# Optimization experiments

Hardware: AMD Instinct MI355X
Metric: run time of the kernel (lower is better)

Reference implementation:

```python
import jax, jax.numpy as jnp
import numpy as np

B, T, V, E, H, K, PAD = 32, 512, 50000, 256, 512, 17, 0


def setup_inputs() -> dict:
    key = jax.random.key(0)
    ks = jax.random.split(key, 16)
    s = 0.05
    input_ids = jax.random.randint(ks[0], (B, T), 1, V)
    lengths = jax.random.randint(ks[1], (B,), T // 2, T + 1)  # >=1 token, mask[:,0] all True
    tags = jax.random.randint(ks[2], (B, T), 0, K)
    mask = jnp.arange(T)[None, :] < lengths[:, None]
    emb = (jax.random.normal(ks[3], (V, E)) * s).at[PAD].set(0.0)  # padding_idx row zeroed
    w_ih_f = jax.random.normal(ks[4], (4 * H, E)) * s
    w_hh_f = jax.random.normal(ks[5], (4 * H, H)) * s
    b_f = jax.random.normal(ks[6], (4 * H,)) * s
    w_ih_b = jax.random.normal(ks[7], (4 * H, E)) * s
    w_hh_b = jax.random.normal(ks[8], (4 * H, H)) * s
    b_b = jax.random.normal(ks[9], (4 * H,)) * s
    w_cls = jax.random.normal(ks[10], (K, 2 * H)) * s
    b_cls = jax.random.normal(ks[11], (K,)) * s
    start_trans = jax.random.normal(ks[12], (K,)) * s
    trans = jax.random.normal(ks[13], (K, K)) * s
    end_trans = jax.random.normal(ks[14], (K,)) * s
    return dict(input_ids=input_ids, lengths=lengths, tags=tags, mask=mask,
                emb=emb, w_ih_f=w_ih_f, w_hh_f=w_hh_f, b_f=b_f,
                w_ih_b=w_ih_b, w_hh_b=w_hh_b, b_b=b_b,
                w_cls=w_cls, b_cls=b_cls,
                start_trans=start_trans, trans=trans, end_trans=end_trans)


def _lstm(xg, w_hh):
    # xg: [B,T,4H] = x @ W_ih^T + b (precomputed); scan adds recurrent term.
    Bq, Hq = xg.shape[0], w_hh.shape[1]

    def step(carry, g_in):
        h, c = carry
        g = g_in + h @ w_hh.T
        i, f, gg, o = jnp.split(g, 4, axis=-1)  # torch gate order i,f,g,o
        c = jax.nn.sigmoid(f) * c + jax.nn.sigmoid(i) * jnp.tanh(gg)
        h = jax.nn.sigmoid(o) * jnp.tanh(c)
        return (h, c), h

    init = (jnp.zeros((Bq, Hq), xg.dtype), jnp.zeros((Bq, Hq), xg.dtype))
    _, hs = jax.lax.scan(step, init, jnp.swapaxes(xg, 0, 1))
    return jnp.swapaxes(hs, 0, 1)  # [B,T,H]


def _forward_math(input_ids, lengths, tags, mask, emb,
                  w_ih_f, w_hh_f, b_f, w_ih_b, w_hh_b, b_b,
                  w_cls, b_cls, start_trans, trans, end_trans):
    x = emb[input_ids]  # [B,T,E]
    # forward direction over padded seq (valid prefix is causally correct)
    hf = _lstm(x @ w_ih_f.T + b_f, w_hh_f)
    # backward direction: reverse each sequence within its own length (packed semantics)
    t = jnp.arange(input_ids.shape[1])[None, :]
    rev = jnp.where(t < lengths[:, None], lengths[:, None] - 1 - t, t)  # involution on valid region
    xr = jnp.take_along_axis(x, rev[:, :, None], axis=1)
    hb = _lstm(xr @ w_ih_b.T + b_b, w_hh_b)
    hb = jnp.take_along_axis(hb, rev[:, :, None], axis=1)
    enc = jnp.concatenate([hf, hb], axis=-1)  # dropout = identity (eval / p=0)
    emissions = enc @ w_cls.T + b_cls  # [B,T,K]
    m = mask.astype(emissions.dtype)
    # ---- CRF numerator (gold path score) ----
    emis_sc = jnp.sum(jnp.take_along_axis(emissions, tags[:, :, None], axis=2)[..., 0] * m, axis=1)
    tr_sc = jnp.sum(trans[tags[:, :-1], tags[:, 1:]] * m[:, 1:], axis=1)
    last_tag = jnp.take_along_axis(tags, (lengths - 1)[:, None], axis=1)[:, 0]
    numer = start_trans[tags[:, 0]] + emis_sc + tr_sc + end_trans[last_tag]
    # ---- CRF partition (forward algorithm) ----
    def fstep(alpha, inp):
        e_t, m_t = inp
        nxt = jax.nn.logsumexp(alpha[:, :, None] + trans[None, :, :] + e_t[:, None, :], axis=1)
        return jnp.where(m_t[:, None], nxt, alpha), None

    alpha0 = start_trans[None, :] + emissions[:, 0]
    alphaT, _ = jax.lax.scan(
        fstep, alpha0,
        (jnp.swapaxes(emissions[:, 1:], 0, 1), jnp.swapaxes(mask[:, 1:], 0, 1)))
    logZ = jax.nn.logsumexp(alphaT + end_trans[None, :], axis=1)
    return -jnp.mean(numer - logZ)  # reduction='mean', negated


def reference(input_ids, lengths, tags, mask, emb, w_ih_f, w_hh_f, b_f,
              w_ih_b, w_hh_b, b_b, w_cls, b_cls, start_trans, trans, end_trans):
    return _forward_math(input_ids, lengths, tags, mask, emb, w_ih_f, w_hh_f, b_f,
                         w_ih_b, w_hh_b, b_b, w_cls, b_cls, start_trans, trans, end_trans)
```

## Files before the change

### kernel.cpp

```cpp
#include <hip/hip_runtime.h>
#include <hip/hip_bf16.h>
#include <stdint.h>

#define B_  32
#define T_  512
#define E_  256
#define H_  512
#define K_  17

typedef unsigned short us;
typedef __attribute__((ext_vector_type(8))) short short8;
typedef __attribute__((ext_vector_type(4))) float f32x4;

__device__ __forceinline__ float bf2f(unsigned int u16) {
    union { unsigned int i; float f; } v; v.i = u16 << 16; return v.f;
}
__device__ __forceinline__ us f2bf(float f) {
    union { float f; unsigned int i; } v; v.f = f;
    unsigned int b = v.i;
    return (us)((b + 0x7FFFu + ((b >> 16) & 1u)) >> 16);
}
__device__ __forceinline__ float sigf(float x) { return 1.0f / (1.0f + __expf(-x)); }
__device__ __forceinline__ float tanhf_(float x) { return 1.0f - 2.0f / (__expf(2.0f * x) + 1.0f); }

__global__ void k_cvt(const float* __restrict__ src, us* __restrict__ dst, int n4) {
    int i = blockIdx.x * 256 + threadIdx.x;
    if (i < n4) {
        float4 v = ((const float4*)src)[i];
        uint2 p;
        p.x = (uint32_t)f2bf(v.x) | ((uint32_t)f2bf(v.y) << 16);
        p.y = (uint32_t)f2bf(v.z) | ((uint32_t)f2bf(v.w) << 16);
        ((uint2*)dst)[i] = p;
    }
}

__global__ void k_init(const int* __restrict__ ids, const int* __restrict__ lengths,
                       int* __restrict__ ids2, int* __restrict__ marker,
                       int* __restrict__ flags, float* __restrict__ out) {
    int idx = blockIdx.x * 256 + threadIdx.x;
    if (idx == 0) { *marker = 1; out[0] = -3328.0f; }
    if (idx < 1024) flags[idx] = 0;
    if (idx < 2 * B_ * T_) {
        int dir = idx >> 14;
        int r   = idx & 16383;
        int t   = r >> 5;
        int b   = r & 31;
        int l   = lengths[b];
        int tt  = (dir == 0) ? t : ((t < l) ? (l - 1 - t) : t);
        ids2[idx] = ids[b * T_ + tt];
    }
}

__launch_bounds__(256)
__global__ void k_xg(const us* __restrict__ emb,
                     const us* __restrict__ wf, const float* __restrict__ bfv,
                     const us* __restrict__ wb, const float* __restrict__ bbv,
                     const int* __restrict__ ids2, us* __restrict__ xg,
                     int* __restrict__ marker) {
    if (blockIdx.x == 0 && blockIdx.y == 0 && blockIdx.z == 0 && threadIdx.x == 0)
        atomicOr(marker, 2);
    int mt = blockIdx.x, nt = blockIdx.y, dir = blockIdx.z;
    const us* W      = dir ? wb  : wf;
    const float* bias = dir ? bbv : bfv;
    const int* id2 = ids2 + dir * (B_ * T_);
    us* xgd = xg + (size_t)dir * B_ * T_ * 2048;
    int m0 = mt * 64, n0 = nt * 64;
    __shared__ __align__(16) us As[64][136];
    __shared__ __align__(16) us Bs[64][136];
    int tid = threadIdx.x;
    int wv = tid >> 6, lane = tid & 63;
    int lm = lane & 15, lg = lane >> 4;
    f32x4 z = {0.f, 0.f, 0.f, 0.f};
    f32x4 acc[4] = {z, z, z, z};
    for (int half = 0; half < 2; ++half) {
        for (int c = tid; c < 1024; c += 256) {
            int row = c >> 4, cb = c & 15;
            int mg = m0 + row;
            int j = mg >> 2, g = mg & 3;
            *(uint4*)&As[row][cb * 8] =
                *(const uint4*)(W + ((size_t)(g * H_ + j)) * E_ + half * 128 + cb * 8);
            int gi = id2[n0 + row];
            *(uint4*)&Bs[row][cb * 8] =
                *(const uint4*)(emb + (size_t)gi * E_ + half * 128 + cb * 8);
        }
        __syncthreads();
#pragma unroll
        for (int kt = 0; kt < 4; ++kt) {
            short8 a = *(const short8*)&As[wv * 16 + lm][kt * 32 + lg * 8];
#pragma unroll
            for (int n2 = 0; n2 < 4; ++n2) {
                short8 b = *(const short8*)&Bs[n2 * 16 + lm][kt * 32 + lg * 8];
                acc[n2] = __builtin_amdgcn_mfma_f32_16x16x32_bf16(a, b, acc[n2], 0, 0, 0);
            }
        }
        __syncthreads();
    }
    int jgb = m0 + wv * 16 + lg * 4;
    int j = jgb >> 2;
#pragma unroll
    for (int n2 = 0; n2 < 4; ++n2) {
        int token = n0 + n2 * 16 + lm;
        us p[4];
#pragma unroll
        for (int q = 0; q < 4; ++q)
            p[q] = f2bf(acc[n2][q] + bias[q * H_ + j]);
        uint2 pv;
        pv.x = (uint32_t)p[0] | ((uint32_t)p[1] << 16);
        pv.y = (uint32_t)p[2] | ((uint32_t)p[3] << 16);
        *(uint2*)(xgd + (size_t)token * 2048 + jgb) = pv;
    }
}

__launch_bounds__(256)
__global__ void k_lstm(const us* __restrict__ whf, const us* __restrict__ whb,
                       const us* __restrict__ xg,
                       us* __restrict__ h_state, us* __restrict__ h_out,
                       int* __restrict__ flags, int* __restrict__ marker) {
    int bid = blockIdx.x;
    int dir = bid >> 5, w = bid & 31;
    int tid = threadIdx.x;
    if (bid == 0 && tid == 0) atomicOr(marker, 4);
    const us* Wg = dir ? whb : whf;
    __shared__ __align__(16) us Ws[64 * 512];
    __shared__ __align__(4)  us Hx[32 * 16];
    for (int c = tid; c < 4096; c += 256) {
        int row = c >> 6, cb = c & 63;
        int rt = row >> 4, rl = row & 15;
        int jj = rl >> 2, g = rl & 3;
        int srcRow = g * H_ + w * 16 + rt * 4 + jj;
        uint4 v = *(const uint4*)(Wg + (size_t)srcRow * H_ + cb * 8);
        int lb = row * 1024 + ((cb * 16) ^ ((row & 7) << 4));
        *(uint4*)((char*)Ws + lb) = v;
    }
    __syncthreads();
    int wv = tid >> 6, lane = tid & 63;
    int nb = wv & 1, rh = wv >> 1;
    int lm = lane & 15, lg = lane >> 4;
    int b = nb * 16 + lm;
    const us* xgd = xg + (size_t)dir * B_ * T_ * 2048;
    us* hod = h_out + (size_t)dir * B_ * T_ * H_;
    int* slots = flags + dir * 512;
    const uint64_t* hbase = (const uint64_t*)h_state + (size_t)dir * 8192;
    uint32_t* hw32 = (uint32_t*)h_state + (size_t)dir * 16384;
    float cc0 = 0.f, cc1 = 0.f;
    bool alive = true;
#pragma unroll 1
    for (int t = 0; t < T_; ++t) {
        f32x4 acc[2];
#pragma unroll
        for (int ti = 0; ti < 2; ++ti) {
            int jl = rh * 8 + ti * 4 + lg;
            uint2 v = *(const uint2*)(xgd + ((size_t)(t * 32 + b)) * 2048 + (w * 16 + jl) * 4);
            acc[ti][0] = bf2f(v.x & 0xffff); acc[ti][1] = bf2f(v.x >> 16);
            acc[ti][2] = bf2f(v.y & 0xffff); acc[ti][3] = bf2f(v.y >> 16);
        }
        if (t > 0) {
            if (wv == 0) {
                int polls = 0;
                for (;;) {
                    int v = (lane < 32)
                        ? __hip_atomic_load(&slots[lane * 16], __ATOMIC_RELAXED, __HIP_MEMORY_SCOPE_AGENT)
                        : 0x7fffffff;
                    if (__all(v >= t) || !alive) break;
                    __builtin_amdgcn_s_sleep(1);
                    if (++polls > 300000) {
                        if (lane == 0) atomicOr(marker, 32);
                        alive = false;
                    }
                }
            }
            __syncthreads();
            const uint64_t* hp = hbase + ((t - 1) & 1) * 4096 + (size_t)b * 128 + lg * 2;
            uint64_t hv[32];
#pragma unroll
            for (int kt = 0; kt < 16; ++kt) {
                hv[2 * kt]     = __hip_atomic_load(hp + kt * 8,     __ATOMIC_RELAXED, __HIP_MEMORY_SCOPE_AGENT);
                hv[2 * kt + 1] = __hip_atomic_load(hp + kt * 8 + 1, __ATOMIC_RELAXED, __HIP_MEMORY_SCOPE_AGENT);
            }
#pragma unroll
            for (int ti = 0; ti < 2; ++ti) {
                int r0 = (rh * 2 + ti) * 16 + lm;
                const char* abase = (const char*)Ws + r0 * 1024;
                int sw = (r0 & 7) << 4;
#pragma unroll
                for (int kt = 0; kt < 16; ++kt) {
                    union { uint64_t u[2]; short8 s; } bu;
                    bu.u[0] = hv[2 * kt]; bu.u[1] = hv[2 * kt + 1];
                    short8 a = *(const short8*)(abase + ((kt * 64 + lg * 16) ^ sw));
                    acc[ti] = __builtin_amdgcn_mfma_f32_16x16x32_bf16(a, bu.s, acc[ti], 0, 0, 0);
                }
            }
        }
        {
            float ci = cc0;
            ci = sigf(acc[0][1]) * ci + sigf(acc[0][0]) * tanhf_(acc[0][2]);
            float h = sigf(acc[0][3]) * tanhf_(ci);
            cc0 = ci;
            us hv = f2bf(h);
            int jl = rh * 8 + lg;
            Hx[b * 16 + jl] = hv;
            hod[((size_t)b * T_ + t) * H_ + w * 16 + jl] = hv;
        }
        {
            float ci = cc1;
            ci = sigf(acc[1][1]) * ci + sigf(acc[1][0]) * tanhf_(acc[1][2]);
            float h = sigf(acc[1][3]) * tanhf_(ci);
            cc1 = ci;
            us hv = f2bf(h);
            int jl = rh * 8 + 4 + lg;
            Hx[b * 16 + jl] = hv;
            hod[((size_t)b * T_ + t) * H_ + w * 16 + jl] = hv;
        }
        __syncthreads();
        {
            uint32_t v = ((const uint32_t*)Hx)[tid];
            int bb = tid >> 3, jp = tid & 7;
            atomicExch(&hw32[(size_t)(t & 1) * 8192 + (size_t)bb * 256 + w * 8 + jp], v);
        }
        __syncthreads();
        if (tid == 0) atomicExch(&slots[w * 16], t + 1);
    }
}

__launch_bounds__(256)
__global__ void k_emis(const us* __restrict__ h_out,
                       const us* __restrict__ wcls, const float* __restrict__ bcls,
                       const int* __restrict__ lengths, float* __restrict__ emis,
                       int* __restrict__ marker) {
    if (blockIdx.x == 0 && threadIdx.x == 0) atomicOr(marker, 8);
    __shared__ __align__(8) us Wc[17][1032];
    int tid = threadIdx.x;
    for (int c = tid; c < 17 * 256; c += 256) {
        int row = c >> 8; int c4 = (c & 255) * 4;
        *(uint2*)&Wc[row][c4] = *(const uint2*)(wcls + (size_t)row * 1024 + c4);
    }
    __syncthreads();
    int i = blockIdx.x * 8 + (tid >> 5);
    int k = tid & 31;
    int b = i >> 9, t = i & 511;
    int l = lengths[b];
    int trv = (t < l) ? (l - 1 - t) : t;
    const us* hf = h_out + ((size_t)(0 * B_ + b) * T_ + t) * H_;
    const us* hb = h_out + ((size_t)(1 * B_ + b) * T_ + trv) * H_;
    if (k < K_) {
        float acc = bcls[k];
        for (int e = 0; e < H_; e += 4) {
            uint2 hv = *(const uint2*)(hf + e);
            uint2 wv = *(const uint2*)&Wc[k][e];
            acc = fmaf(bf2f(hv.x & 0xffff), bf2f(wv.x & 0xffff), acc);
            acc = fmaf(bf2f(hv.x >> 16),    bf2f(wv.x >> 16),    acc);
            acc = fmaf(bf2f(hv.y & 0xffff), bf2f(wv.y & 0xffff), acc);
            acc = fmaf(bf2f(hv.y >> 16),    bf2f(wv.y >> 16),    acc);
        }
        for (int e = 0; e < H_; e += 4) {
            uint2 hv = *(const uint2*)(hb + e);
            uint2 wv = *(const uint2*)&Wc[k][512 + e];
            acc = fmaf(bf2f(hv.x & 0xffff), bf2f(wv.x & 0xffff), acc);
            acc = fmaf(bf2f(hv.x >> 16),    bf2f(wv.x >> 16),    acc);
            acc = fmaf(bf2f(hv.y & 0xffff), bf2f(wv.y & 0xffff), acc);
            acc = fmaf(bf2f(hv.y >> 16),    bf2f(wv.y >> 16),    acc);
        }
        emis[(size_t)i * 20 + k] = acc;
    }
}

__global__ void k_crf(const float* __restrict__ emis, const int* __restrict__ tags,
                      const int* __restrict__ lengths,
                      const float* __restrict__ start_t, const float* __restrict__ trans_t,
                      const float* __restrict__ end_t, float* __restrict__ res,
                      int* __restrict__ marker) {
    if (blockIdx.x == 0 && threadIdx.x == 0) atomicOr(marker, 16);
    __shared__ float tr[17][18];
    __shared__ float alpha[17];
    int b = blockIdx.x, tid = threadIdx.x;
    for (int i = tid; i < 289; i += 64) tr[i / 17][i % 17] = trans_t[i];
    __syncthreads();
    int l = lengths[b];
    const int* tg = tags + b * T_;
    const float* eb = emis + (size_t)b * T_ * 20;
    float sn = 0.f;
    for (int t = tid; t < T_; t += 64) {
        if (t < l) {
            sn += eb[t * 20 + tg[t]];
            if (t >= 1) sn += tr[tg[t - 1]][tg[t]];
        }
    }
#pragma unroll
    for (int off = 32; off; off >>= 1) sn += __shfl_xor(sn, off, 64);
    float numer = sn + start_t[tg[0]] + end_t[tg[l - 1]];
    int k = (tid < K_) ? tid : 0;
    if (tid < K_) alpha[tid] = start_t[tid] + eb[tid];
    __syncthreads();
    for (int t = 1; t < l; ++t) {
        float av[17];
        float m = -1e30f;
#pragma unroll
        for (int j = 0; j < 17; ++j) { av[j] = alpha[j] + tr[j][k]; m = fmaxf(m, av[j]); }
        float s = 0.f;
#pragma unroll
        for (int j = 0; j < 17; ++j) s += __expf(av[j] - m);
        float nxt = m + __logf(s) + eb[t * 20 + k];
        __syncthreads();
        if (tid < K_) alpha[tid] = nxt;
        __syncthreads();
    }
    float v = (tid < K_) ? (alpha[tid] + end_t[tid]) : -1e30f;
    float m2 = v;
#pragma unroll
    for (int off = 32; off; off >>= 1) m2 = fmaxf(m2, __shfl_xor(m2, off, 64));
    float s2 = __expf(v - m2);
#pragma unroll
    for (int off = 32; off; off >>= 1) s2 += __shfl_xor(s2, off, 64);
    if (tid == 0) res[b] = numer - (m2 + __logf(s2));
}

__global__ void k_fin(const float* __restrict__ res, int* __restrict__ marker,
                      int hostmask, float* __restrict__ out) {
    int tid = threadIdx.x;
    if (hostmask != 0) {
        if (tid == 0) out[0] = -(16384.0f + 512.0f * (float)hostmask);
        return;
    }
    int dm = atomicOr(marker, 0);
    if (dm != 31) {
        if (tid == 0) out[0] = -(8192.0f + 128.0f * (float)(dm & 63));
        return;
    }
    float v = (tid < B_) ? res[tid] : 0.f;
    unsigned long long nb = __ballot(v != v);
    if (nb != 0ULL) {
        if (tid == 0) out[0] = -(4096.0f + (float)(__ffsll((long long)nb) - 1));
        return;
    }
#pragma unroll
    for (int off = 32; off; off >>= 1) v += __shfl_xor(v, off, 64);
    if (tid == 0) out[0] = -(v / (float)B_);
}

extern "C" void kernel_launch(void* const* d_in, const int* in_sizes, int n_in,
                              void* d_out, int out_size, void* d_ws, size_t ws_size,
                              hipStream_t stream) {
    const int* ids      = (const int*)d_in[0];
    const int* lengths  = (const int*)d_in[1];
    const int* tags     = (const int*)d_in[2];
    const float* emb_f  = (const float*)d_in[4];
    const float* wihf_f = (const float*)d_in[5];
    const float* whhf_f = (const float*)d_in[6];
    const float* bfv    = (const float*)d_in[7];
    const float* wihb_f = (const float*)d_in[8];
    const float* whhb_f = (const float*)d_in[9];
    const float* bbv    = (const float*)d_in[10];
    const float* wcls_f = (const float*)d_in[11];
    const float* bcls   = (const float*)d_in[12];
    const float* start  = (const float*)d_in[13];
    const float* trans  = (const float*)d_in[14];
    const float* endt   = (const float*)d_in[15];
    float* out = (float*)d_out;

    int hm = 0;
    if (n_in != 16 || out_size != 1) hm |= 8;
    const int exp_sz[16] = {
        16384, 32, 16384, 16384,
        12800000,
        524288, 1048576, 2048,
        524288, 1048576, 2048,
        17408, 17,
        17, 289, 17
    };
    if (!(hm & 8))
        for (int i = 0; i < 16; ++i)
            if (in_sizes[i] != exp_sz[i]) hm |= 2;

    char* w = (char*)d_ws;
    size_t off = 0;
    auto carve = [&](size_t bytes) { void* p = w + off; off += (bytes + 255) & ~(size_t)255; return p; };
    int* ids2    = (int*)carve((size_t)2 * B_ * T_ * 4);
    int* marker  = (int*)carve(256);
    int* flags   = (int*)carve(4096);
    float* res   = (float*)carve(256);
    float* emis  = (float*)carve((size_t)B_ * T_ * 20 * 4);
    us* xg       = (us*)carve((size_t)2 * B_ * T_ * 2048 * 2);
    us* h_st     = (us*)carve((size_t)2 * 2 * B_ * H_ * 2);
    us* h_out    = (us*)carve((size_t)2 * B_ * T_ * H_ * 2);
    us* emb_b    = (us*)carve((size_t)12800000 * 2);
    us* wihf_b   = (us*)carve((size_t)524288 * 2);
    us* wihb_b   = (us*)carve((size_t)524288 * 2);
    us* whhf_b   = (us*)carve((size_t)1048576 * 2);
    us* whhb_b   = (us*)carve((size_t)1048576 * 2);
    us* wcls_b   = (us*)carve((size_t)17408 * 2);
    if (off > ws_size) hm |= 4;

    (void)hipGetLastError();
    if ((hm & (2 | 4 | 8)) == 0) {
        k_init<<<(2 * B_ * T_ + 255) / 256, 256, 0, stream>>>(ids, lengths, ids2, marker, flags, out);
        k_cvt<<<(12800000 / 4 + 255) / 256, 256, 0, stream>>>(emb_f,  emb_b,  12800000 / 4);
        k_cvt<<<(524288   / 4 + 255) / 256, 256, 0, stream>>>(wihf_f, wihf_b, 524288 / 4);
        k_cvt<<<(524288   / 4 + 255) / 256, 256, 0, stream>>>(wihb_f, wihb_b, 524288 / 4);
        k_cvt<<<(1048576  / 4 + 255) / 256, 256, 0, stream>>>(whhf_f, whhf_b, 1048576 / 4);
        k_cvt<<<(1048576  / 4 + 255) / 256, 256, 0, stream>>>(whhb_f, whhb_b, 1048576 / 4);
        k_cvt<<<(17408    / 4 + 255) / 256, 256, 0, stream>>>(wcls_f, wcls_b, 17408 / 4);
        k_xg<<<dim3(2048 / 64, B_ * T_ / 64, 2), 256, 0, stream>>>(emb_b, wihf_b, bfv, wihb_b, bbv, ids2, xg, marker);
        k_lstm<<<64, 256, 0, stream>>>(whhf_b, whhb_b, xg, h_st, h_out, flags, marker);
        k_emis<<<B_ * T_ / 8, 256, 0, stream>>>(h_out, wcls_b, bcls, lengths, emis, marker);
        k_crf<<<B_, 64, 0, stream>>>(emis, tags, lengths, start, trans, endt, res, marker);
        if (hipGetLastError() != hipSuccess) hm |= 1;
    }
    k_fin<<<1, 64, 0, stream>>>(res, marker, hm, out);
}
```

Measured before the change: 3.066 ms.

## Cut per-step barriers in LSTM handoff and CRF recurrence using shuffles

In the persistent LSTM kernel, the shared-memory staging buffer and one of the two block barriers per timestep are removed. Lanes pair adjacent bf16 outputs through a wave shuffle and publish them straight to the global h exchange buffer with relaxed atomic stores. The flag update becomes a release store, and the xg gate-input loads are issued before the poll/wait so their latency overlaps it. The CRF forward recurrence keeps alpha in registers, broadcast by shuffle, with transition columns in registers, which removes two barriers per step. The risk is that memory ordering now rests on the release store after a single barrier.

After: 3.896 ms. +27.1%, slower.

```diff
diff --git a/kernel.cpp b/kernel.cpp
--- a/kernel.cpp
+++ b/kernel.cpp
@@ -122,7 +122,6 @@
     if (bid == 0 && tid == 0) atomicOr(marker, 4);
     const us* Wg = dir ? whb : whf;
     __shared__ __align__(16) us Ws[64 * 512];
-    __shared__ __align__(4)  us Hx[32 * 16];
     for (int c = tid; c < 4096; c += 256) {
         int row = c >> 6, cb = c & 63;
         int rt = row >> 4, rl = row & 15;
@@ -137,6 +136,8 @@
     int nb = wv & 1, rh = wv >> 1;
     int lm = lane & 15, lg = lane >> 4;
     int b = nb * 16 + lm;
+    int jl0 = rh * 8 + lg;
+    int jl1 = rh * 8 + 4 + lg;
     const us* xgd = xg + (size_t)dir * B_ * T_ * 2048;
     us* hod = h_out + (size_t)dir * B_ * T_ * H_;
     int* slots = flags + dir * 512;
@@ -146,14 +147,9 @@
     bool alive = true;
 #pragma unroll 1
     for (int t = 0; t < T_; ++t) {
+        uint2 vr0 = *(const uint2*)(xgd + ((size_t)(t * 32 + b)) * 2048 + (w * 16 + jl0) * 4);
+        uint2 vr1 = *(const uint2*)(xgd + ((size_t)(t * 32 + b)) * 2048 + (w * 16 + jl1) * 4);
         f32x4 acc[2];
-#pragma unroll
-        for (int ti = 0; ti < 2; ++ti) {
-            int jl = rh * 8 + ti * 4 + lg;
-            uint2 v = *(const uint2*)(xgd + ((size_t)(t * 32 + b)) * 2048 + (w * 16 + jl) * 4);
-            acc[ti][0] = bf2f(v.x & 0xffff); acc[ti][1] = bf2f(v.x >> 16);
-            acc[ti][2] = bf2f(v.y & 0xffff); acc[ti][3] = bf2f(v.y >> 16);
-        }
         if (t > 0) {
             if (wv == 0) {
                 int polls = 0;
@@ -177,6 +173,10 @@
                 hv[2 * kt]     = __hip_atomic_load(hp + kt * 8,     __ATOMIC_RELAXED, __HIP_MEMORY_SCOPE_AGENT);
                 hv[2 * kt + 1] = __hip_atomic_load(hp + kt * 8 + 1, __ATOMIC_RELAXED, __HIP_MEMORY_SCOPE_AGENT);
             }
+            acc[0][0] = bf2f(vr0.x & 0xffff); acc[0][1] = bf2f(vr0.x >> 16);
+            acc[0][2] = bf2f(vr0.y & 0xffff); acc[0][3] = bf2f(vr0.y >> 16);
+            acc[1][0] = bf2f(vr1.x & 0xffff); acc[1][1] = bf2f(vr1.x >> 16);
+            acc[1][2] = bf2f(vr1.y & 0xffff); acc[1][3] = bf2f(vr1.y >> 16);
 #pragma unroll
             for (int ti = 0; ti < 2; ++ti) {
                 int r0 = (rh * 2 + ti) * 16 + lm;
@@ -190,35 +190,31 @@
                     acc[ti] = __builtin_amdgcn_mfma_f32_16x16x32_bf16(a, bu.s, acc[ti], 0, 0, 0);
                 }
             }
-        }
-        {
-            float ci = cc0;
-            ci = sigf(acc[0][1]) * ci + sigf(acc[0][0]) * tanhf_(acc[0][2]);
-            float h = sigf(acc[0][3]) * tanhf_(ci);
-            cc0 = ci;
-            us hv = f2bf(h);
-            int jl = rh * 8 + lg;
-            Hx[b * 16 + jl] = hv;
-            hod[((size_t)b * T_ + t) * H_ + w * 16 + jl] = hv;
-        }
-        {
-            float ci = cc1;
-            ci = sigf(acc[1][1]) * ci + sigf(acc[1][0]) * tanhf_(acc[1][2]);
-            float h = sigf(acc[1][3]) * tanhf_(ci);
-            cc1 = ci;
-            us hv = f2bf(h);
-            int jl = rh * 8 + 4 + lg;
-            Hx[b * 16 + jl] = hv;
-            hod[((size_t)b * T_ + t) * H_ + w * 16 + jl] = hv;
+        } else {
+            acc[0][0] = bf2f(vr0.x & 0xffff); acc[0][1] = bf2f(vr0.x >> 16);
+            acc[0][2] = bf2f(vr0.y & 0xffff); acc[0][3] = bf2f(vr0.y >> 16);
+            acc[1][0] = bf2f(vr1.x & 0xffff); acc[1][1] = bf2f(vr1.x >> 16);
+            acc[1][2] = bf2f(vr1.y & 0xffff); acc[1][3] = bf2f(vr1.y >> 16);
+        }
+        cc0 = sigf(acc[0][1]) * cc0 + sigf(acc[0][0]) * tanhf_(acc[0][2]);
+        float h0 = sigf(acc[0][3]) * tanhf_(cc0);
+        cc1 = sigf(acc[1][1]) * cc1 + sigf(acc[1][0]) * tanhf_(acc[1][2]);
+        float h1 = sigf(acc[1][3]) * tanhf_(cc1);
+        us p0 = f2bf(h0), p1 = f2bf(h1);
+        hod[((size_t)b * T_ + t) * H_ + w * 16 + jl0] = p0;
+        hod[((size_t)b * T_ + t) * H_ + w * 16 + jl1] = p1;
+        int y0 = __shfl((int)p0, lane + 16);
+        int y1 = __shfl((int)p1, lane + 16);
+        if ((lg & 1) == 0) {
+            uint32_t u0 = (uint32_t)p0 | ((uint32_t)(us)y0 << 16);
+            uint32_t u1 = (uint32_t)p1 | ((uint32_t)(us)y1 << 16);
+            uint32_t* hwp = hw32 + (size_t)(t & 1) * 8192 + (size_t)b * 256 + w * 8 + rh * 4 + (lg >> 1);
+            __hip_atomic_store(hwp,     u0, __ATOMIC_RELAXED, __HIP_MEMORY_SCOPE_AGENT);
+            __hip_atomic_store(hwp + 2, u1, __ATOMIC_RELAXED, __HIP_MEMORY_SCOPE_AGENT);
         }
         __syncthreads();
-        {
-            uint32_t v = ((const uint32_t*)Hx)[tid];
-            int bb = tid >> 3, jp = tid & 7;
-            atomicExch(&hw32[(size_t)(t & 1) * 8192 + (size_t)bb * 256 + w * 8 + jp], v);
-        }
-        __syncthreads();
-        if (tid == 0) atomicExch(&slots[w * 16], t + 1);
+        if (tid == 0)
+            __hip_atomic_store(&slots[w * 16], t + 1, __ATOMIC_RELEASE, __HIP_MEMORY_SCOPE_AGENT);
     }
 }
 
@@ -271,7 +267,6 @@
                       int* __restrict__ marker) {
     if (blockIdx.x == 0 && threadIdx.x == 0) atomicOr(marker, 16);
     __shared__ float tr[17][18];
-    __shared__ float alpha[17];
     int b = blockIdx.x, tid = threadIdx.x;
     for (int i = tid; i < 289; i += 64) tr[i / 17][i % 17] = trans_t[i];
     __syncthreads();
@@ -288,23 +283,25 @@
 #pragma unroll
     for (int off = 32; off; off >>= 1) sn += __shfl_xor(sn, off, 64);
     float numer = sn + start_t[tg[0]] + end_t[tg[l - 1]];
-    int k = (tid < K_) ? tid : 0;
-    if (tid < K_) alpha[tid] = start_t[tid] + eb[tid];
-    __syncthreads();
+    int k = (tid < K_) ? tid : (K_ - 1);
+    float trc[17];
+#pragma unroll
+    for (int j = 0; j < 17; ++j) trc[j] = trans_t[j * 17 + k];
+    float alpha = start_t[k] + eb[k];
     for (int t = 1; t < l; ++t) {
         float av[17];
         float m = -1e30f;
 #pragma unroll
-        for (int j = 0; j < 17; ++j) { av[j] = alpha[j] + tr[j][k]; m = fmaxf(m, av[j]); }
+        for (int j = 0; j < 17; ++j) {
+            av[j] = __shfl(alpha, j) + trc[j];
+            m = fmaxf(m, av[j]);
+        }
         float s = 0.f;
 #pragma unroll
         for (int j = 0; j < 17; ++j) s += __expf(av[j] - m);
-        float nxt = m + __logf(s) + eb[t * 20 + k];
-        __syncthreads();
-        if (tid < K_) alpha[tid] = nxt;
-        __syncthreads();
-    }
-    float v = (tid < K_) ? (alpha[tid] + end_t[tid]) : -1e30f;
+        alpha = m + __logf(s) + eb[t * 20 + k];
+    }
+    float v = (tid < K_) ? (alpha + end_t[tid]) : -1e30f;
     float m2 = v;
 #pragma unroll
     for (int off = 32; off; off >>= 1) m2 = fmaxf(m2, __shfl_xor(m2, off, 64));
```
